# Kernel optimization log

Hardware: AMD Instinct MI355X
Metric: run time of the kernel (lower is better)

Reference implementation:

```python
import jax, jax.numpy as jnp
import numpy as np

H, C, OC, WIN = 12, 768, 768, 4
HD = C // H  # 64
B, T = 4, 1024


def setup_inputs() -> dict:
    key = jax.random.key(0)
    ks = jax.random.split(key, 8)
    s = C ** -0.5  # xavier-ish scale for 1x1 convs
    rel_s = HD ** -0.5
    return {
        "x": jax.random.normal(ks[0], (B, C, T), jnp.float32),
        "c": jax.random.normal(ks[1], (B, C, T), jnp.float32),
        "mask": jnp.ones((B, 1, T, T), jnp.float32),
        "wq": jax.random.normal(ks[2], (C, C), jnp.float32) * s,
        "bq": jnp.zeros((C,), jnp.float32),
        "wk": jax.random.normal(ks[3], (C, C), jnp.float32) * s,
        "bk": jnp.zeros((C,), jnp.float32),
        "wv": jax.random.normal(ks[4], (C, C), jnp.float32) * s,
        "bv": jnp.zeros((C,), jnp.float32),
        "wo": jax.random.normal(ks[5], (OC, C), jnp.float32) * s,
        "bo": jnp.zeros((OC,), jnp.float32),
        "emb_rel_k": jax.random.normal(ks[6], (H, 2 * WIN + 1, HD), jnp.float32) * rel_s,
        "emb_rel_v": jax.random.normal(ks[7], (H, 2 * WIN + 1, HD), jnp.float32) * rel_s,
    }


def _conv1x1(x, w, b):
    # Conv1d(kernel_size=1): pointwise linear over channels. x:(b,c,t) w:(o,c)
    return jnp.einsum('oc,bct->bot', w, x) + b[None, :, None]


def _get_rel_emb(emb, t):
    pad = max(t - WIN, 0)
    start = max(WIN + 1 - t, 0)
    emb = jnp.pad(emb, ((0, 0), (pad, pad), (0, 0)))
    return emb[:, start:start + 2 * t - 1, :]


def _rel_to_abs(x):
    # (b,h,t,2t-1) -> (b,h,t,t) via the pad/reshape skew trick
    b, h, t, _ = x.shape
    x = jnp.pad(x, ((0, 0), (0, 0), (0, 0), (0, 1))).reshape(b, h, 2 * t * t)
    x = jnp.pad(x, ((0, 0), (0, 0), (0, t - 1))).reshape(b, h, t + 1, 2 * t - 1)
    return x[:, :, :t, t - 1:]


def _abs_to_rel(x):
    # (b,h,t,t) -> (b,h,t,2t-1) via inverse skew trick
    b, h, t, _ = x.shape
    x = jnp.pad(x, ((0, 0), (0, 0), (0, 0), (0, t - 1))).reshape(b, h, t * (2 * t - 1))
    x = jnp.pad(x, ((0, 0), (0, 0), (t, 0))).reshape(b, h, t, 2 * t)
    return x[:, :, :, 1:]


def reference(x, c, mask, wq, bq, wk, bk, wv, bv, wo, bo, emb_rel_k, emb_rel_v):
    b, _, t = x.shape
    scale = HD ** -0.5
    # (b,c,t) -> (b,h,t,hd)
    q = _conv1x1(x, wq, bq).reshape(b, H, HD, t).transpose(0, 1, 3, 2)
    k = _conv1x1(c, wk, bk).reshape(b, H, HD, t).transpose(0, 1, 3, 2)
    v = _conv1x1(c, wv, bv).reshape(b, H, HD, t).transpose(0, 1, 3, 2)
    scores = jnp.einsum('bhqd,bhkd->bhqk', q, k) * scale  # (b,h,t,t)
    rel_k = _get_rel_emb(emb_rel_k, t)                    # (h,2t-1,d)
    rel_logits = jnp.einsum('bhtd,hmd->bhtm', q, rel_k)   # (b,h,t,2t-1)
    scores = scores + _rel_to_abs(rel_logits) * scale
    scores = jnp.where(mask == 0, jnp.float32(-1e4), scores)
    attn = jax.nn.softmax(scores, axis=-1)
    out = jnp.einsum('bhqk,bhkd->bhqd', attn, v)
    rel_v = _get_rel_emb(emb_rel_v, t)
    out = out + jnp.einsum('bhtm,hmd->bhtd', _abs_to_rel(attn), rel_v)
    out = out.transpose(0, 1, 3, 2).reshape(b, C, t)      # (b,c,t)
    return _conv1x1(out, wo, bo)
```

## Files before the change

### kernel.cpp

```cpp
#include <hip/hip_runtime.h>
#include <stdint.h>
#include <stddef.h>

#define B_ 4
#define T_ 1024
#define C_ 768
#define H_ 12
#define QSCALE 0.18033688011112042f
#define MASKPEN -14427.0f

typedef __attribute__((ext_vector_type(4))) float f32x4;
typedef __attribute__((ext_vector_type(8))) short s16x8;
typedef __attribute__((ext_vector_type(4))) float float4v;

typedef const __attribute__((address_space(1))) uint32_t ga_u32;
typedef __attribute__((address_space(3))) uint32_t lds_u32;

__device__ __forceinline__ float bf2f(uint16_t u) {
    union { uint32_t u; float f; } cv; cv.u = ((uint32_t)u) << 16; return cv.f;
}
__device__ __forceinline__ uint16_t f2bf(float f) {
    union { float f; uint32_t u; } cv; cv.f = f;
    uint32_t u = cv.u;
    return (uint16_t)((u + 0x7FFFu + ((u >> 16) & 1u)) >> 16);
}
__device__ __forceinline__ uint16_t f2bf_trunc(float f) {
    union { float f; uint32_t u; } cv; cv.f = f;
    return (uint16_t)(cv.u >> 16);
}
__device__ __forceinline__ void gload16(const uint16_t* g, uint16_t* l) {
    __builtin_amdgcn_global_load_lds((ga_u32*)g, (lds_u32*)l, 16, 0, 0);
}

__global__ void transpose_bf16_kernel(const float* __restrict__ x,
                                      const float* __restrict__ c,
                                      uint16_t* __restrict__ xT,
                                      uint16_t* __restrict__ cT) {
    __shared__ float tile[32][33];
    const int which = blockIdx.z;
    const int b = blockIdx.y;
    const int t0 = (blockIdx.x % (T_ / 32)) * 32;
    const int c0 = (blockIdx.x / (T_ / 32)) * 32;
    const float* src = (which ? c : x) + (size_t)b * C_ * T_;
    uint16_t* dst = (which ? cT : xT) + (size_t)b * T_ * C_;
    const int lj = threadIdx.x & 31, li = threadIdx.x >> 5;
    #pragma unroll
    for (int i = li; i < 32; i += 8)
        tile[i][lj] = src[(size_t)(c0 + i) * T_ + t0 + lj];
    __syncthreads();
    #pragma unroll
    for (int i = li; i < 32; i += 8)
        dst[(size_t)(t0 + i) * C_ + c0 + lj] = f2bf(tile[lj][i]);
}

__global__ void convert_weights_kernel(const float* __restrict__ wq,
                                       const float* __restrict__ wk,
                                       const float* __restrict__ wv,
                                       const float* __restrict__ wo,
                                       uint16_t* __restrict__ out) {
    const int which = blockIdx.y;
    const float* w = (which == 0) ? wq : (which == 1) ? wk : (which == 2) ? wv : wo;
    const float sc = (which == 0) ? QSCALE : 1.0f;
    uint16_t* dst = out + (size_t)which * C_ * C_;
    const int i = (blockIdx.x * 256 + threadIdx.x) * 4;
    float4v v = *(const float4v*)(w + i);
    uint32_t lo = (uint32_t)f2bf(v[0] * sc) | ((uint32_t)f2bf(v[1] * sc) << 16);
    uint32_t hi = (uint32_t)f2bf(v[2] * sc) | ((uint32_t)f2bf(v[3] * sc) << 16);
    uint32_t* d32 = (uint32_t*)(dst + i);
    d32[0] = lo; d32[1] = hi;
}

__global__ void convert_ek_kernel(const float* __restrict__ ek,
                                  uint16_t* __restrict__ ekb) {
    const int i = blockIdx.x * 256 + threadIdx.x;
    ekb[i] = f2bf(ek[i]);
}

__global__ void mask_bits_kernel(const float* __restrict__ mask,
                                 uint32_t* __restrict__ bits) {
    const size_t i = (size_t)blockIdx.x * 256 + threadIdx.x;
    const float m = mask[i];
    unsigned long long bal = __ballot(m != 0.0f);
    const int lane = threadIdx.x & 63;
    if (lane == 0)       bits[i >> 5] = (uint32_t)bal;
    else if (lane == 32) bits[i >> 5] = (uint32_t)(bal >> 32);
}

__global__ void mask_flags_kernel(const uint32_t* __restrict__ bits,
                                  uint32_t* __restrict__ flags) {
    const int b = blockIdx.y, i0 = blockIdx.x * 64;
    const uint32_t* p = bits + ((size_t)b * T_ + i0) * 32;
    bool ok = true;
    #pragma unroll
    for (int it = 0; it < 8; ++it) ok &= (p[it * 256 + threadIdx.x] == 0xFFFFFFFFu);
    __shared__ int s_ok[4];
    const bool wall = __all(ok);
    if ((threadIdx.x & 63) == 0) s_ok[threadIdx.x >> 6] = wall ? 1 : 0;
    __syncthreads();
    if (threadIdx.x == 0)
        flags[b * 16 + blockIdx.x] = (uint32_t)(s_ok[0] & s_ok[1] & s_ok[2] & s_ok[3]);
}

template <bool OPROJ>
__global__ __launch_bounds__(256, 2)
void gemm_kernel(const uint16_t* __restrict__ xT, const uint16_t* __restrict__ cT,
                 const uint16_t* __restrict__ wb,
                 const float* __restrict__ bq, const float* __restrict__ bk,
                 const float* __restrict__ bv, const float* __restrict__ bo,
                 const uint16_t* __restrict__ attT,
                 uint16_t* __restrict__ Qb, uint16_t* __restrict__ Kb,
                 uint16_t* __restrict__ Vb, float* __restrict__ outp) {
    const int tid = threadIdx.x;
    const int z = blockIdx.z;

    const uint16_t* A; const uint16_t* Bm; const float* bias;
    uint16_t* Cb = nullptr; float* Cf = nullptr;
    int N, ldc; bool bias_col; float bscale = 1.0f;
    if (!OPROJ) {
        const int bat = z & 3, which = z >> 2;
        if (which == 0) {
            A = xT + (size_t)bat * T_ * C_; Bm = wb;                bias = bq;
            Cb = Qb + (size_t)bat * T_ * C_; N = C_; ldc = C_; bias_col = true;
            bscale = QSCALE;
        } else if (which == 1) {
            A = cT + (size_t)bat * T_ * C_; Bm = wb + 1 * C_ * C_;  bias = bk;
            Cb = Kb + (size_t)bat * T_ * C_; N = C_; ldc = C_; bias_col = true;
        } else {
            A = wb + 2 * (size_t)C_ * C_;   Bm = cT + (size_t)(z & 3) * T_ * C_; bias = bv;
            Cb = Vb + (size_t)bat * C_ * T_; N = T_; ldc = T_; bias_col = false;
        }
    } else {
        A = wb + 3 * (size_t)C_ * C_; Bm = attT + (size_t)z * T_ * C_; bias = bo;
        Cf = outp + (size_t)z * C_ * T_; N = T_; ldc = T_; bias_col = false;
    }
    const int tn_cnt = N / 128;
    const int tm = blockIdx.x / tn_cnt, tn = blockIdx.x % tn_cnt;
    const int row0 = tm * 128, col0 = tn * 128;

    __shared__ uint16_t As[128 * 64];
    __shared__ uint16_t Bs[128 * 64];

    const int w = tid >> 6, l = tid & 63;
    const int wr = w & 1, wc = w >> 1;

    const f32x4 zz = {0.f, 0.f, 0.f, 0.f};
    f32x4 acc[4][4];
    #pragma unroll
    for (int i = 0; i < 4; ++i)
        #pragma unroll
        for (int j = 0; j < 4; ++j) acc[i][j] = zz;

    const int sr = tid >> 3, sp = tid & 7;

    for (int kt = 0; kt < 12; ++kt) {
        const int k0 = kt * 64;
        #pragma unroll
        for (int it = 0; it < 4; ++it) {
            const int row = it * 32 + sr;
            const int cch = sp ^ (row & 7);
            gload16(A + (size_t)(row0 + row) * 768 + k0 + cch * 8, &As[row * 64 + sp * 8]);
        }
        #pragma unroll
        for (int it = 0; it < 4; ++it) {
            const int row = it * 32 + sr;
            const int cch = sp ^ (row & 7);
            gload16(Bm + (size_t)(col0 + row) * 768 + k0 + cch * 8, &Bs[row * 64 + sp * 8]);
        }
        __syncthreads();

        #pragma unroll
        for (int kk = 0; kk < 2; ++kk) {
            s16x8 af[4], bf[4];
            #pragma unroll
            for (int i = 0; i < 4; ++i) {
                const int arow = wr * 64 + i * 16 + (l & 15);
                const int ach = (kk * 4 + (l >> 4)) ^ (arow & 7);
                af[i] = *(const s16x8*)(&As[arow * 64 + ach * 8]);
                const int brow = wc * 64 + i * 16 + (l & 15);
                const int bch = (kk * 4 + (l >> 4)) ^ (brow & 7);
                bf[i] = *(const s16x8*)(&Bs[brow * 64 + bch * 8]);
            }
            #pragma unroll
            for (int i = 0; i < 4; ++i)
                #pragma unroll
                for (int j = 0; j < 4; ++j)
                    acc[i][j] = __builtin_amdgcn_mfma_f32_16x16x32_bf16(af[i], bf[j], acc[i][j], 0, 0, 0);
        }
        __syncthreads();
    }

    #pragma unroll
    for (int i = 0; i < 4; ++i) {
        const int rowb = row0 + wr * 64 + i * 16 + ((l >> 4) * 4);
        #pragma unroll
        for (int j = 0; j < 4; ++j) {
            const int col = col0 + wc * 64 + j * 16 + (l & 15);
            const float bc = bias_col ? bias[col] * bscale : 0.f;
            #pragma unroll
            for (int r = 0; r < 4; ++r) {
                const int row = rowb + r;
                const float v = acc[i][j][r] + (bias_col ? bc : bias[row]);
                if (!OPROJ) Cb[(size_t)row * ldc + col] = f2bf(v);
                else        Cf[(size_t)row * ldc + col] = v;
            }
        }
    }
}

__global__ __launch_bounds__(256, 2)
void attn_kernel(const uint16_t* __restrict__ Qb, const uint16_t* __restrict__ Kb,
                 const uint16_t* __restrict__ Vb, const uint32_t* __restrict__ mbits,
                 const uint32_t* __restrict__ flags,
                 const uint16_t* __restrict__ ekb, const float* __restrict__ emb_v,
                 uint16_t* __restrict__ attT) {
    const int i0 = blockIdx.x * 64;
    const int h = blockIdx.y, b = blockIdx.z;
    const int tid = threadIdx.x, w = tid >> 6, l = tid & 63;

    __shared__ uint16_t Ks[2][64 * 64];
    __shared__ uint16_t Vs[2][64 * 64];
    __shared__ uint16_t Ps[64 * 72];
    __shared__ uint16_t Es[16 * 72];
    __shared__ float rk[64 * 9];
    __shared__ float sband[64 * 9];

    const uint16_t* Kbase = Kb + (size_t)b * T_ * C_ + h * 64;
    const uint16_t* Vbase = Vb + (size_t)b * C_ * T_ + (size_t)(h * 64) * T_;
    const int sr = tid >> 3, sp = tid & 7;

    auto stage = [&](int jt, int buf) {
        const int j0s = jt * 64;
        #pragma unroll
        for (int it = 0; it < 2; ++it) {
            const int row = it * 32 + sr;
            const int cch = sp ^ (row & 7);
            gload16(Kbase + (size_t)(j0s + row) * C_ + cch * 8, &Ks[buf][row * 64 + sp * 8]);
        }
        #pragma unroll
        for (int it = 0; it < 2; ++it) {
            const int row = it * 32 + sr;
            const int cch = sp ^ (row & 7);
            gload16(Vbase + (size_t)row * T_ + j0s + cch * 8, &Vs[buf][row * 64 + sp * 8]);
        }
    };

    stage(0, 0);

    s16x8 qf[2];
    {
        const int row = i0 + w * 16 + (l & 15);
        const uint16_t* qp = Qb + ((size_t)(b * T_ + row)) * C_ + h * 64 + (l >> 4) * 8;
        qf[0] = *(const s16x8*)(qp);
        qf[1] = *(const s16x8*)(qp + 32);
    }

    {
        const int idx = tid * 4;
        const int row = idx >> 6, col = idx & 63;
        uint64_t val = 0;
        if (row < 9) val = *(const uint64_t*)(ekb + ((size_t)h * 9 + row) * 64 + col);
        *(uint64_t*)&Es[row * 72 + col] = val;
    }
    for (int t = tid; t < 64 * 9; t += 256) sband[t] = -1e30f;
    __syncthreads();

    {
        f32x4 racc = {0.f, 0.f, 0.f, 0.f};
        #pragma unroll
        for (int kk = 0; kk < 2; ++kk) {
            s16x8 ef = *(const s16x8*)(&Es[(l & 15) * 72 + (l >> 4) * 8 + kk * 32]);
            racc = __builtin_amdgcn_mfma_f32_16x16x32_bf16(qf[kk], ef, racc, 0, 0, 0);
        }
        if ((l & 15) < 9) {
            #pragma unroll
            for (int r = 0; r < 4; ++r)
                rk[(w * 16 + (l >> 4) * 4 + r) * 9 + (l & 15)] = racc[r];
        }
    }

    const bool maskones = (flags[b * 16 + blockIdx.x] != 0);
    const uint32_t* mrow = mbits + (size_t)b * T_ * 32;

    float m[4], lsum[4];
    const f32x4 zz = {0.f, 0.f, 0.f, 0.f};
    f32x4 oacc[4] = {zz, zz, zz, zz};
    #pragma unroll
    for (int r = 0; r < 4; ++r) { m[r] = -1e30f; lsum[r] = 0.f; }

    const int iMin = i0 + w * 16, iMax = iMin + 15;

    for (int jt = 0; jt < 16; ++jt) {
        const int cur = jt & 1;
        if (jt < 15) stage(jt + 1, cur ^ 1);
        const int j0 = jt * 64;

        float sv[4][4];
        #pragma unroll
        for (int tn = 0; tn < 4; ++tn) {
            f32x4 s = zz;
            #pragma unroll
            for (int kk = 0; kk < 2; ++kk) {
                const int krow = tn * 16 + (l & 15);
                const int kch = (kk * 4 + (l >> 4)) ^ (krow & 7);
                s16x8 kf = *(const s16x8*)(&Ks[cur][krow * 64 + kch * 8]);
                s = __builtin_amdgcn_mfma_f32_16x16x32_bf16(qf[kk], kf, s, 0, 0, 0);
            }
            #pragma unroll
            for (int r = 0; r < 4; ++r) sv[tn][r] = s[r];
        }

        const bool bandTile = (j0 <= iMax + 5) && (j0 + 63 >= iMin - 3);
        if (bandTile) {
            #pragma unroll
            for (int tn = 0; tn < 4; ++tn)
                #pragma unroll
                for (int r = 0; r < 4; ++r) {
                    const int iloc = w * 16 + (l >> 4) * 4 + r;
                    const int rr = (j0 + tn * 16 + (l & 15)) - (i0 + iloc) + 3;
                    if ((unsigned)rr < 9u) sv[tn][r] += rk[iloc * 9 + rr];
                }
        }
        if (!maskones) {
            #pragma unroll
            for (int r = 0; r < 4; ++r) {
                const int i = i0 + w * 16 + (l >> 4) * 4 + r;
                const uint32_t m0 = mrow[(size_t)i * 32 + (j0 >> 5)];
                const uint32_t m1 = mrow[(size_t)i * 32 + (j0 >> 5) + 1];
                #pragma unroll
                for (int tn = 0; tn < 4; ++tn) {
                    const uint32_t mw = (tn < 2) ? m0 : m1;
                    const int bit = (tn * 16 + (l & 15)) & 31;
                    if (!((mw >> bit) & 1u)) sv[tn][r] = MASKPEN;
                }
            }
        }
        if (bandTile) {
            #pragma unroll
            for (int tn = 0; tn < 4; ++tn)
                #pragma unroll
                for (int r = 0; r < 4; ++r) {
                    const int iloc = w * 16 + (l >> 4) * 4 + r;
                    const int rr = (j0 + tn * 16 + (l & 15)) - (i0 + iloc) + 3;
                    if ((unsigned)rr < 9u) sband[iloc * 9 + rr] = sv[tn][r];
                }
        }

        float mx[4];
        #pragma unroll
        for (int r = 0; r < 4; ++r)
            mx[r] = fmaxf(fmaxf(sv[0][r], sv[1][r]), fmaxf(sv[2][r], sv[3][r]));
        const bool need = (mx[0] > m[0]) | (mx[1] > m[1]) | (mx[2] > m[2]) | (mx[3] > m[3]);
        if (__any(need)) {
            #pragma unroll
            for (int r = 0; r < 4; ++r) {
                float v = mx[r];
                v = fmaxf(v, __shfl_xor(v, 1));
                v = fmaxf(v, __shfl_xor(v, 2));
                v = fmaxf(v, __shfl_xor(v, 4));
                v = fmaxf(v, __shfl_xor(v, 8));
                const float mn = fmaxf(m[r], v);
                const float alpha = exp2f(m[r] - mn);
                m[r] = mn;
                lsum[r] *= alpha;
                #pragma unroll
                for (int td = 0; td < 4; ++td) oacc[td][r] *= alpha;
            }
        }
        #pragma unroll
        for (int r = 0; r < 4; ++r) {
            #pragma unroll
            for (int tn = 0; tn < 4; ++tn) {
                const float p = exp2f(sv[tn][r] - m[r]);
                sv[tn][r] = p;
                lsum[r] += p;
            }
        }

        #pragma unroll
        for (int tn = 0; tn < 4; ++tn)
            #pragma unroll
            for (int r = 0; r < 4; ++r) {
                const int prow = w * 16 + (l >> 4) * 4 + r;
                Ps[prow * 72 + tn * 16 + (l & 15)] = f2bf_trunc(sv[tn][r]);
            }

        #pragma unroll
        for (int ks = 0; ks < 2; ++ks) {
            const int prow = w * 16 + (l & 15);
            s16x8 pf = *(const s16x8*)(&Ps[prow * 72 + ks * 32 + (l >> 4) * 8]);
            #pragma unroll
            for (int td = 0; td < 4; ++td) {
                const int vrow = td * 16 + (l & 15);
                const int vch = (ks * 4 + (l >> 4)) ^ (vrow & 7);
                s16x8 vf = *(const s16x8*)(&Vs[cur][vrow * 64 + vch * 8]);
                oacc[td] = __builtin_amdgcn_mfma_f32_16x16x32_bf16(pf, vf, oacc[td], 0, 0, 0);
            }
        }
        __syncthreads();
    }

    float invl[4];
    #pragma unroll
    for (int r = 0; r < 4; ++r) {
        float s = lsum[r];
        s += __shfl_xor(s, 1);
        s += __shfl_xor(s, 2);
        s += __shfl_xor(s, 4);
        s += __shfl_xor(s, 8);
        invl[r] = 1.f / s;
    }
    float ab[4][9];
    #pragma unroll
    for (int r = 0; r < 4; ++r) {
        const int iloc = w * 16 + (l >> 4) * 4 + r;
        #pragma unroll
        for (int rr = 0; rr < 9; ++rr)
            ab[r][rr] = exp2f(sband[iloc * 9 + rr] - m[r]) * invl[r];
    }
    #pragma unroll
    for (int td = 0; td < 4; ++td) {
        const int d = td * 16 + (l & 15);
        const float* ev = emb_v + (size_t)h * 9 * 64 + d;
        #pragma unroll
        for (int r = 0; r < 4; ++r) {
            float v = oacc[td][r] * invl[r];
            #pragma unroll
            for (int rr = 0; rr < 9; ++rr) v += ab[r][rr] * ev[rr * 64];
            const int i = i0 + w * 16 + (l >> 4) * 4 + r;
            attT[((size_t)(b * T_ + i)) * C_ + h * 64 + d] = f2bf(v);
        }
    }
}

extern "C" void kernel_launch(void* const* d_in, const int* in_sizes, int n_in,
                              void* d_out, int out_size, void* d_ws, size_t ws_size,
                              hipStream_t stream) {
    const float* x    = (const float*)d_in[0];
    const float* c    = (const float*)d_in[1];
    const float* mask = (const float*)d_in[2];
    const float* wq   = (const float*)d_in[3];
    const float* bq   = (const float*)d_in[4];
    const float* wk   = (const float*)d_in[5];
    const float* bk   = (const float*)d_in[6];
    const float* wv   = (const float*)d_in[7];
    const float* bv   = (const float*)d_in[8];
    const float* wo   = (const float*)d_in[9];
    const float* bo   = (const float*)d_in[10];
    const float* ek   = (const float*)d_in[11];
    const float* ev   = (const float*)d_in[12];
    float* out = (float*)d_out;

    uint8_t* ws = (uint8_t*)d_ws;
    size_t off = 0;
    auto alloc = [&](size_t bytes) {
        uint8_t* p = ws + off;
        off += (bytes + 255) & ~(size_t)255;
        return p;
    };
    uint16_t* xT   = (uint16_t*)alloc((size_t)B_ * T_ * C_ * 2);
    uint16_t* cT   = (uint16_t*)alloc((size_t)B_ * T_ * C_ * 2);
    uint16_t* wb   = (uint16_t*)alloc((size_t)4 * C_ * C_ * 2);
    uint16_t* Qb   = (uint16_t*)alloc((size_t)B_ * T_ * C_ * 2);
    uint16_t* Kb   = (uint16_t*)alloc((size_t)B_ * T_ * C_ * 2);
    uint16_t* Vb   = (uint16_t*)alloc((size_t)B_ * C_ * T_ * 2);
    uint16_t* attT = (uint16_t*)alloc((size_t)B_ * T_ * C_ * 2);
    uint32_t* mbits = (uint32_t*)alloc((size_t)B_ * T_ * 32 * 4);
    uint16_t* ekb  = (uint16_t*)alloc((size_t)H_ * 9 * 64 * 2);
    uint32_t* mflags = (uint32_t*)alloc((size_t)B_ * 16 * 4);

    transpose_bf16_kernel<<<dim3(768, B_, 2), 256, 0, stream>>>(x, c, xT, cT);
    convert_weights_kernel<<<dim3(576, 4), 256, 0, stream>>>(wq, wk, wv, wo, wb);
    convert_ek_kernel<<<dim3(27), 256, 0, stream>>>(ek, ekb);
    mask_bits_kernel<<<dim3((B_ * T_ * T_) / 256), 256, 0, stream>>>(mask, mbits);
    mask_flags_kernel<<<dim3(16, B_), 256, 0, stream>>>(mbits, mflags);
    gemm_kernel<false><<<dim3(48, 1, 12), 256, 0, stream>>>(xT, cT, wb, bq, bk, bv, bo,
                                                            attT, Qb, Kb, Vb, out);
    attn_kernel<<<dim3(T_ / 64, H_, B_), 256, 0, stream>>>(Qb, Kb, Vb, mbits, mflags,
                                                           ekb, ev, attT);
    gemm_kernel<true><<<dim3(48, 1, 4), 256, 0, stream>>>(xT, cT, wb, bq, bk, bv, bo,
                                                          attT, Qb, Kb, Vb, out);
}
```

Before: 220.9 us.

## Double-buffer GEMM tiles, vectorize transpose, remap attention grid and raise occupancy

The projection GEMM now double-buffers its LDS tiles so global-to-LDS loads for the next K step overlap MFMA work on the current one. The input transpose uses float4 loads and packed 64-bit bf16 stores. The attention kernel switches to a 1D grid that groups query tiles of the same batch-head for cache locality, asks for three blocks per CU, and raises wave priority around its MFMA sections. These trade more LDS and register pressure for overlap and occupancy, and risk spills from the tighter launch bounds.

```diff
diff --git a/kernel.cpp b/kernel.cpp
--- a/kernel.cpp
+++ b/kernel.cpp
@@ -39,18 +39,20 @@
     __shared__ float tile[32][33];
     const int which = blockIdx.z;
     const int b = blockIdx.y;
-    const int t0 = (blockIdx.x % (T_ / 32)) * 32;
-    const int c0 = (blockIdx.x / (T_ / 32)) * 32;
+    const int t0 = (blockIdx.x & 31) * 32;
+    const int c0 = (blockIdx.x >> 5) * 32;
     const float* src = (which ? c : x) + (size_t)b * C_ * T_;
     uint16_t* dst = (which ? cT : xT) + (size_t)b * T_ * C_;
-    const int lj = threadIdx.x & 31, li = threadIdx.x >> 5;
-    #pragma unroll
-    for (int i = li; i < 32; i += 8)
-        tile[i][lj] = src[(size_t)(c0 + i) * T_ + t0 + lj];
+    const int li = threadIdx.x >> 3, lj4 = (threadIdx.x & 7) * 4;
+    float4v v = *(const float4v*)(src + (size_t)(c0 + li) * T_ + t0 + lj4);
+    tile[li][lj4 + 0] = v[0]; tile[li][lj4 + 1] = v[1];
+    tile[li][lj4 + 2] = v[2]; tile[li][lj4 + 3] = v[3];
     __syncthreads();
-    #pragma unroll
-    for (int i = li; i < 32; i += 8)
-        dst[(size_t)(t0 + i) * C_ + c0 + lj] = f2bf(tile[lj][i]);
+    const uint64_t pk = (uint64_t)f2bf(tile[lj4 + 0][li])
+                      | ((uint64_t)f2bf(tile[lj4 + 1][li]) << 16)
+                      | ((uint64_t)f2bf(tile[lj4 + 2][li]) << 32)
+                      | ((uint64_t)f2bf(tile[lj4 + 3][li]) << 48);
+    *(uint64_t*)(dst + (size_t)(t0 + li) * C_ + c0 + lj4) = pk;
 }
 
 __global__ void convert_weights_kernel(const float* __restrict__ wq,
@@ -137,8 +139,8 @@
     const int tm = blockIdx.x / tn_cnt, tn = blockIdx.x % tn_cnt;
     const int row0 = tm * 128, col0 = tn * 128;
 
-    __shared__ uint16_t As[128 * 64];
-    __shared__ uint16_t Bs[128 * 64];
+    __shared__ uint16_t As[2][128 * 64];
+    __shared__ uint16_t Bs[2][128 * 64];
 
     const int w = tid >> 6, l = tid & 63;
     const int wr = w & 1, wc = w >> 1;
@@ -152,21 +154,28 @@
 
     const int sr = tid >> 3, sp = tid & 7;
 
-    for (int kt = 0; kt < 12; ++kt) {
+    auto stage = [&](int kt, int buf) {
         const int k0 = kt * 64;
         #pragma unroll
         for (int it = 0; it < 4; ++it) {
             const int row = it * 32 + sr;
             const int cch = sp ^ (row & 7);
-            gload16(A + (size_t)(row0 + row) * 768 + k0 + cch * 8, &As[row * 64 + sp * 8]);
+            gload16(A + (size_t)(row0 + row) * 768 + k0 + cch * 8, &As[buf][row * 64 + sp * 8]);
         }
         #pragma unroll
         for (int it = 0; it < 4; ++it) {
             const int row = it * 32 + sr;
             const int cch = sp ^ (row & 7);
-            gload16(Bm + (size_t)(col0 + row) * 768 + k0 + cch * 8, &Bs[row * 64 + sp * 8]);
-        }
-        __syncthreads();
+            gload16(Bm + (size_t)(col0 + row) * 768 + k0 + cch * 8, &Bs[buf][row * 64 + sp * 8]);
+        }
+    };
+
+    stage(0, 0);
+    __syncthreads();
+
+    for (int kt = 0; kt < 12; ++kt) {
+        const int cur = kt & 1;
+        if (kt < 11) stage(kt + 1, cur ^ 1);
 
         #pragma unroll
         for (int kk = 0; kk < 2; ++kk) {
@@ -175,10 +184,10 @@
             for (int i = 0; i < 4; ++i) {
                 const int arow = wr * 64 + i * 16 + (l & 15);
                 const int ach = (kk * 4 + (l >> 4)) ^ (arow & 7);
-                af[i] = *(const s16x8*)(&As[arow * 64 + ach * 8]);
+                af[i] = *(const s16x8*)(&As[cur][arow * 64 + ach * 8]);
                 const int brow = wc * 64 + i * 16 + (l & 15);
                 const int bch = (kk * 4 + (l >> 4)) ^ (brow & 7);
-                bf[i] = *(const s16x8*)(&Bs[brow * 64 + bch * 8]);
+                bf[i] = *(const s16x8*)(&Bs[cur][brow * 64 + bch * 8]);
             }
             #pragma unroll
             for (int i = 0; i < 4; ++i)
@@ -207,14 +216,17 @@
     }
 }
 
-__global__ __launch_bounds__(256, 2)
+__global__ __launch_bounds__(256, 3)
 void attn_kernel(const uint16_t* __restrict__ Qb, const uint16_t* __restrict__ Kb,
                  const uint16_t* __restrict__ Vb, const uint32_t* __restrict__ mbits,
                  const uint32_t* __restrict__ flags,
                  const uint16_t* __restrict__ ekb, const float* __restrict__ emb_v,
                  uint16_t* __restrict__ attT) {
-    const int i0 = blockIdx.x * 64;
-    const int h = blockIdx.y, b = blockIdx.z;
+    const int n = blockIdx.x;
+    const int qt = (n >> 3) & 15;
+    const int bh = (n & 7) + 8 * (n >> 7);
+    const int b = bh / 12, h = bh % 12;
+    const int i0 = qt * 64;
     const int tid = threadIdx.x, w = tid >> 6, l = tid & 63;
 
     __shared__ uint16_t Ks[2][64 * 64];
@@ -278,7 +290,7 @@
         }
     }
 
-    const bool maskones = (flags[b * 16 + blockIdx.x] != 0);
+    const bool maskones = (flags[b * 16 + qt] != 0);
     const uint32_t* mrow = mbits + (size_t)b * T_ * 32;
 
     float m[4], lsum[4];
@@ -295,6 +307,7 @@
         const int j0 = jt * 64;
 
         float sv[4][4];
+        __builtin_amdgcn_s_setprio(1);
         #pragma unroll
         for (int tn = 0; tn < 4; ++tn) {
             f32x4 s = zz;
@@ -308,6 +321,7 @@
             #pragma unroll
             for (int r = 0; r < 4; ++r) sv[tn][r] = s[r];
         }
+        __builtin_amdgcn_s_setprio(0);
 
         const bool bandTile = (j0 <= iMax + 5) && (j0 + 63 >= iMin - 3);
         if (bandTile) {
@@ -384,6 +398,7 @@
                 Ps[prow * 72 + tn * 16 + (l & 15)] = f2bf_trunc(sv[tn][r]);
             }
 
+        __builtin_amdgcn_s_setprio(1);
         #pragma unroll
         for (int ks = 0; ks < 2; ++ks) {
             const int prow = w * 16 + (l & 15);
@@ -396,6 +411,7 @@
                 oacc[td] = __builtin_amdgcn_mfma_f32_16x16x32_bf16(pf, vf, oacc[td], 0, 0, 0);
             }
         }
+        __builtin_amdgcn_s_setprio(0);
         __syncthreads();
     }
 
@@ -475,8 +491,7 @@
     mask_flags_kernel<<<dim3(16, B_), 256, 0, stream>>>(mbits, mflags);
     gemm_kernel<false><<<dim3(48, 1, 12), 256, 0, stream>>>(xT, cT, wb, bq, bk, bv, bo,
                                                             attT, Qb, Kb, Vb, out);
-    attn_kernel<<<dim3(T_ / 64, H_, B_), 256, 0, stream>>>(Qb, Kb, Vb, mbits, mflags,
-                                                           ekb, ev, attT);
+    attn_kernel<<<dim3(768), 256, 0, stream>>>(Qb, Kb, Vb, mbits, mflags, ekb, ev, attT);
     gemm_kernel<true><<<dim3(48, 1, 4), 256, 0, stream>>>(xT, cT, wb, bq, bk, bv, bo,
                                                           attT, Qb, Kb, Vb, out);
 }
```

After: 226.0 us. 1.02x slower.
